# Performance work log

Hardware: AMD Instinct MI355X
Metric: run time of the kernel (lower is better)

## Reference

```python
import jax, jax.numpy as jnp
import numpy as np

# PointCNN layer dims
N, NUM_PTS, P, K, DIMS = 32, 2048, 1024, 16, 3
C_IN, C_OUT = 64, 128
C_HALF = C_OUT // 2            # dense lift of raw features
C_MID = C_OUT // 4             # lifted coord features (C_in != 0)
DM = min(int(np.ceil(C_OUT / C_IN)), 4)   # depth multiplier = 2
C_CAT = C_MID + C_HALF         # 96 channels into X-transform matmul
BN_INV = 1.0 / float(np.sqrt(1.0 + 1e-5))  # inference BN, running mean 0 / var 1


def _dense(x, W, b, g, be):
    # Dense = Linear -> ELU -> BatchNorm (inference affine)
    return g * (jax.nn.elu(x @ W + b) * BN_INV) + be


def setup_inputs() -> dict:
    key = jax.random.key(0)
    ks = jax.random.split(key, 24)
    def rn(k, shape, s=0.1):
        return (jax.random.normal(k, shape) * s).astype(jnp.float32)
    return {
        "rep_pts": jax.random.normal(ks[0], (N, P, DIMS), jnp.float32),
        "pts": jax.random.normal(ks[1], (N, NUM_PTS, DIMS), jnp.float32),
        "fts": jax.random.normal(ks[2], (N, NUM_PTS, C_IN), jnp.float32),
        "pts_idx": jax.random.randint(ks[3], (N, P, K), 0, NUM_PTS, dtype=jnp.int32),
        # PointCNN.dense : C_in -> C_out//2
        "d0_W": rn(ks[4], (C_IN, C_HALF)), "d0_b": rn(ks[5], (C_HALF,)),
        "d0_g": jnp.ones((C_HALF,), jnp.float32), "d0_be": rn(ks[6], (C_HALF,)),
        # XConv.dense1 : dims -> C_mid
        "d1_W": rn(ks[7], (DIMS, C_MID)), "d1_b": rn(ks[8], (C_MID,)),
        "d1_g": jnp.ones((C_MID,), jnp.float32), "d1_be": rn(ks[9], (C_MID,)),
        # XConv.dense2 : C_mid -> C_mid
        "d2_W": rn(ks[10], (C_MID, C_MID)), "d2_b": rn(ks[11], (C_MID,)),
        "d2_g": jnp.ones((C_MID,), jnp.float32), "d2_be": rn(ks[12], (C_MID,)),
        # x_trans: Conv2d(dims -> K*K, kernel (1,K)) then 2 Dense (no BN)
        "xc_W": rn(ks[13], (K * K, DIMS, K)), "xc_b": rn(ks[14], (K * K,)),
        "xd1_W": rn(ks[15], (K * K, K * K)), "xd1_b": rn(ks[16], (K * K,)),
        "xd2_W": rn(ks[17], (K * K, K * K)), "xd2_b": rn(ks[18], (K * K,)),
        # end_conv: depthwise (1,K) conv + pointwise conv + ELU + BN
        "dw_W": rn(ks[19], (C_CAT, DM, K)), "dw_b": rn(ks[20], (C_CAT * DM,)),
        "pw_W": rn(ks[21], (C_CAT * DM, C_OUT)), "pw_b": rn(ks[22], (C_OUT,)),
        "end_g": jnp.ones((C_OUT,), jnp.float32), "end_be": rn(ks[23], (C_OUT,)),
    }


def reference(rep_pts, pts, fts, pts_idx, d0_W, d0_b, d0_g, d0_be,
              d1_W, d1_b, d1_g, d1_be, d2_W, d2_b, d2_g, d2_be,
              xc_W, xc_b, xd1_W, xd1_b, xd2_W, xd2_b,
              dw_W, dw_b, pw_W, pw_b, end_g, end_be):
    # lift raw features: Dense C_in -> C_out//2
    fts_l = _dense(fts, d0_W, d0_b, d0_g, d0_be)          # (N, NUM_PTS, C_half)
    # select_region: per-batch irregular neighbor gather
    gather = jax.vmap(lambda a, i: a[i])
    pts_reg = gather(pts, pts_idx)                        # (N,P,K,dims)
    fts_reg = gather(fts_l, pts_idx)                      # (N,P,K,C_half)
    pts_local = pts_reg - rep_pts[:, :, None, :]          # center on rep point
    # lifting MLP on local coordinates
    h = _dense(pts_local, d1_W, d1_b, d1_g, d1_be)
    h = _dense(h, d2_W, d2_b, d2_g, d2_be)                # (N,P,K,C_mid)
    fts_cat = jnp.concatenate([h, fts_reg], axis=-1)      # (N,P,K,C_cat)
    # learned X-transform: Conv2d(dims->K*K, (1,K)) collapses K -> 1, then 2 Dense
    X = jax.nn.elu(jnp.einsum('npkd,qdk->npq', pts_local, xc_W) + xc_b)
    X = jax.nn.elu(X @ xd1_W + xd1_b)
    X = (X @ xd2_W + xd2_b).reshape(pts.shape[0], P, K, K)
    fts_X = jnp.einsum('npij,npjc->npic', X, fts_cat)     # (N,P,K,C_cat)
    # depthwise (groups=C_cat, kernel (1,K)) -> channel layout c*DM+m
    dw = jnp.einsum('npkc,cmk->npcm', fts_X, dw_W)
    dw = dw.reshape(pts.shape[0], P, C_CAT * DM) + dw_b
    # pointwise conv + ELU + inference BN, squeeze collapsed K axis
    out = jax.nn.elu(dw @ pw_W + pw_b)
    return end_g * (out * BN_INV) + end_be                # (N,P,C_out)
```

## Files before the change

### kernel.cpp

```cpp
#include <hip/hip_runtime.h>
#include <hip/hip_bf16.h>
#include <math.h>

#define NBATCH 32
#define NUMPT 2048
#define PP 1024
#define MPB 16
#define BN_INV 0.9999950000374996f

typedef __attribute__((ext_vector_type(8))) short short8;
typedef __attribute__((ext_vector_type(4))) short short4v;
typedef __attribute__((ext_vector_type(4))) float f32x4;

#define MFMA(a,b,c) __builtin_amdgcn_mfma_f32_16x16x32_bf16(a,b,c,0,0,0)

#define FTSL_ELEMS 4194304
#define OFF_D0F  0
#define OFF_XCF  4096
#define OFF_X1F  20480
#define OFF_X2F  86016
#define OFF_D2F  151552
#define OFF_PWF  152576

#define PB0 4096
#define PB1 16384
#define PB2 81920
#define PB3 147456
#define PB4 148480
#define PB5 173056
#define PB6 177152
#define NDB 512
#define NPREP 660

#define CATP 1552

static __device__ __forceinline__ float eluf(float x) {
    return x > 0.0f ? x : (__expf(x) - 1.0f);
}
static __device__ __forceinline__ short f2bf(float x) {
    union { float f; unsigned u; } v; v.f = x;
    unsigned r = v.u + 0x7FFFu + ((v.u >> 16) & 1u);
    return (short)(r >> 16);
}
static __device__ __forceinline__ int f2bf2i(float a, float b) {
    __hip_bfloat162 h = __float22bfloat162_rn(make_float2(a, b));
    int r; __builtin_memcpy(&r, &h, 4); return r;
}
union U8 { short8 s; int i[4]; };
union U4 { short4v s; int i[2]; };

__global__ __launch_bounds__(256) void k_setup(
    const float* __restrict__ fts, const float* __restrict__ d0W,
    const float* __restrict__ xcW, const float* __restrict__ xd1W,
    const float* __restrict__ xd2W, const float* __restrict__ d2W,
    const float* __restrict__ pwW,
    const float* __restrict__ b, const float* __restrict__ g,
    const float* __restrict__ be,
    short* __restrict__ wf, short* __restrict__ fl)
{
    const int tid = threadIdx.x;
    if (blockIdx.x >= NDB) {
        const int gid = PB0 + (blockIdx.x - NDB) * 256 + tid;
        if (gid >= PB6) return;
        float val; int k, n, nt, off;
        if (gid < PB1) {
            int s = gid - PB0;
            n = s / 48; k = s - n * 48; nt = 16; off = OFF_XCF;
            val = xcW[s];
        } else if (gid < PB2) {
            int s = gid - PB1;
            k = s >> 8; n = s & 255; nt = 16; off = OFF_X1F;
            val = xd1W[s];
        } else if (gid < PB3) {
            int s = gid - PB2;
            k = s >> 8; n = s & 255; nt = 16; off = OFF_X2F;
            val = xd2W[s];
        } else if (gid < PB4) {
            int s = gid - PB3;
            k = s >> 5; n = s & 31; nt = 2; off = OFF_D2F;
            val = d2W[s];
        } else if (gid < PB5) {
            int s = gid - PB4;
            k = s >> 7; n = s & 127; nt = 8; off = OFF_PWF;
            val = pwW[s];
        } else {
            int s = gid - PB5;
            k = 48 + (s >> 8); n = s & 255; nt = 16; off = OFF_XCF;
            val = 0.0f;
        }
        const int dst = off + (((k >> 5) * nt + (n >> 4)) * 64
                               + ((k >> 3) & 3) * 16 + (n & 15)) * 8 + (k & 7);
        wf[dst] = f2bf(val);
        return;
    }

    __shared__ __align__(16) short sB[2 * 4160];
    __shared__ __align__(16) short sW0[4096];
    const long base = (long)blockIdx.x * 128 * 64;

    {
        const int k = tid >> 2, n0 = (tid & 3) * 16;
        #pragma unroll
        for (int i4 = 0; i4 < 4; ++i4) {
            float4 v = *(const float4*)&d0W[k * 64 + n0 + i4 * 4];
            float vv[4] = {v.x, v.y, v.z, v.w};
            #pragma unroll
            for (int u = 0; u < 4; ++u) {
                int n = n0 + i4 * 4 + u;
                sW0[(((k >> 5) * 4 + (n >> 4)) * 64 + ((k >> 3) & 3) * 16 + (n & 15)) * 8 + (k & 7)]
                    = f2bf(vv[u]);
            }
        }
    }

    #pragma unroll
    for (int it = 0; it < 4; ++it) {
        const int gidx = tid + it * 256;
        const int r = gidx >> 3, o = gidx & 7;
        float4 va = *(const float4*)&fts[base + r * 64 + o * 8];
        float4 vb = *(const float4*)&fts[base + r * 64 + o * 8 + 4];
        U8 pk;
        pk.i[0] = f2bf2i(va.x, va.y); pk.i[1] = f2bf2i(va.z, va.w);
        pk.i[2] = f2bf2i(vb.x, vb.y); pk.i[3] = f2bf2i(vb.z, vb.w);
        *(short8*)&sB[(o >> 2) * 4160 + (r >> 4) * 520 + ((o & 3) * 16 + (r & 15)) * 8] = pk.s;
    }
    __syncthreads();

    const int wave = tid >> 6, lane = tid & 63;
    const int col = lane & 15, quad = lane >> 4;
    const f32x4 fz = {0.f, 0.f, 0.f, 0.f};
    f32x4 acc[2][4] = {{fz, fz, fz, fz}, {fz, fz, fz, fz}};
    #pragma unroll
    for (int kt = 0; kt < 2; ++kt) {
        short8 af[4];
        #pragma unroll
        for (int mt = 0; mt < 4; ++mt)
            af[mt] = *(const short8*)&sW0[((kt * 4 + mt) * 64 + lane) * 8];
        #pragma unroll
        for (int ni = 0; ni < 2; ++ni) {
            short8 bf_ = *(const short8*)&sB[kt * 4160 + (wave * 2 + ni) * 520 + lane * 8];
            #pragma unroll
            for (int mt = 0; mt < 4; ++mt)
                acc[ni][mt] = MFMA(af[mt], bf_, acc[ni][mt]);
        }
    }
    #pragma unroll
    for (int mt = 0; mt < 4; ++mt) {
        const int c0 = mt * 16 + quad * 4;
        float4 b4 = *(const float4*)&b[c0];
        float4 g4 = *(const float4*)&g[c0];
        float4 e4 = *(const float4*)&be[c0];
        g4.x *= BN_INV; g4.y *= BN_INV; g4.z *= BN_INV; g4.w *= BN_INV;
        #pragma unroll
        for (int ni = 0; ni < 2; ++ni) {
            long rowg = (long)blockIdx.x * 128 + (wave * 2 + ni) * 16 + col;
            U4 sv;
            sv.i[0] = f2bf2i(g4.x * eluf(acc[ni][mt][0] + b4.x) + e4.x,
                             g4.y * eluf(acc[ni][mt][1] + b4.y) + e4.y);
            sv.i[1] = f2bf2i(g4.z * eluf(acc[ni][mt][2] + b4.z) + e4.z,
                             g4.w * eluf(acc[ni][mt][3] + b4.w) + e4.w);
            *(short4v*)&fl[rowg * 64 + c0] = sv.s;
        }
    }
}

__global__ __launch_bounds__(256) void k_xconv(
    const float* __restrict__ rep_pts, const float* __restrict__ pts,
    const int* __restrict__ pts_idx, const short* __restrict__ fl,
    const short* __restrict__ wf,
    const float* __restrict__ d1W, const float* __restrict__ d1b,
    const float* __restrict__ d1g, const float* __restrict__ d1be,
    const float* __restrict__ d2b, const float* __restrict__ d2g,
    const float* __restrict__ d2be,
    const float* __restrict__ xcb, const float* __restrict__ xd1b,
    const float* __restrict__ xd2b,
    const float* __restrict__ dwW, const float* __restrict__ dwb,
    const float* __restrict__ pwb,
    const float* __restrict__ endg, const float* __restrict__ endbe,
    float* __restrict__ out)
{
    __shared__ __align__(16) short s_catF[MPB * CATP];
    __shared__ __align__(16) short s_big[8448];
    __shared__ __align__(16) short s_X0b[4160];
    __shared__ __align__(16) short s_plF[1024];

    const int tid = threadIdx.x;
    const int wave = tid >> 6, lane = tid & 63;
    const int col = lane & 15, quad = lane >> 4;
    const int n = blockIdx.x >> 6;
    const int pb = (blockIdx.x & 63) * MPB;
    const long prow0 = (long)n * PP + pb;
    short* s_h1F = s_big;
    short* s_X1 = s_big;
    short* s_X2 = s_big + 4160;
    short* s_dwF = s_X0b;
    const f32x4 fz = {0.f, 0.f, 0.f, 0.f};
    const short8 zz = {0, 0, 0, 0, 0, 0, 0, 0};

    for (int i = 768 + tid; i < 1024; i += 256) s_plF[i] = 0;
    const int p0 = tid >> 4, k0 = tid & 15;
    const int idxv = pts_idx[(prow0 + p0) * 16 + k0];
    float x0, x1, x2;
    {
        const float* pp = pts + ((long)n * NUMPT + idxv) * 3;
        const float* rp = rep_pts + (prow0 + p0) * 3;
        x0 = pp[0] - rp[0]; x1 = pp[1] - rp[1]; x2 = pp[2] - rp[2];
        const float v[3] = {x0, x1, x2};
        #pragma unroll
        for (int d = 0; d < 3; ++d) {
            int kk = d * 16 + k0;
            s_plF[((kk >> 5) * 64 + ((kk >> 3) & 3) * 16 + p0) * 8 + (kk & 7)] = f2bf(v[d]);
        }
    }

    short8 gv[8];
    {
        const short8* gp = (const short8*)(fl + ((long)n * NUMPT + idxv) * 64);
        #pragma unroll
        for (int i = 0; i < 8; ++i) gv[i] = gp[i];
    }

    #pragma unroll
    for (int oct = 0; oct < 4; ++oct) {
        U8 v8;
        float zv[8];
        #pragma unroll
        for (int u = 0; u < 8; ++u) {
            int c = oct * 8 + u;
            float z = d1b[c] + x0 * d1W[c] + x1 * d1W[32 + c] + x2 * d1W[64 + c];
            zv[u] = (d1g[c] * BN_INV) * eluf(z) + d1be[c];
        }
        v8.i[0] = f2bf2i(zv[0], zv[1]); v8.i[1] = f2bf2i(zv[2], zv[3]);
        v8.i[2] = f2bf2i(zv[4], zv[5]); v8.i[3] = f2bf2i(zv[6], zv[7]);
        *(short8*)&s_h1F[(p0 * 66 + oct * 16 + k0) * 8] = v8.s;
    }

    {
        const int gbase = p0 * CATP + 32 * 16 + k0;
        #pragma unroll
        for (int i = 0; i < 8; ++i) {
            #pragma unroll
            for (int u = 0; u < 8; ++u)
                s_catF[gbase + (i * 8 + u) * 16] = gv[i][u];
        }
    }
    __syncthreads();

    {
        const short8* B = (const short8*)(wf + OFF_D2F);
        short8 b0 = B[lane], b1 = B[64 + lane];
        short8 a[4];
        #pragma unroll
        for (int mt0 = 0; mt0 < 4; ++mt0)
            a[mt0] = *(const short8*)&s_h1F[((wave * 4 + mt0) * 66 + lane) * 8];
        #pragma unroll
        for (int nb = 0; nb < 2; ++nb) {
            int c2 = nb * 16 + col;
            float bb = d2b[c2], gg = d2g[c2] * BN_INV, bee = d2be[c2];
            #pragma unroll
            for (int mt0 = 0; mt0 < 4; ++mt0) {
                int mt = wave * 4 + mt0;
                f32x4 acc = MFMA(a[mt0], nb ? b1 : b0, fz);
                U4 sv;
                sv.i[0] = f2bf2i(gg * eluf(acc[0] + bb) + bee,
                                 gg * eluf(acc[1] + bb) + bee);
                sv.i[1] = f2bf2i(gg * eluf(acc[2] + bb) + bee,
                                 gg * eluf(acc[3] + bb) + bee);
                *(short4v*)&s_catF[mt * CATP + c2 * 16 + quad * 4] = sv.s;
            }
        }
    }

    {
        short8 a0 = *(const short8*)&s_plF[lane * 8];
        short8 a1 = *(const short8*)&s_plF[(64 + lane) * 8];
        const short8* B = (const short8*)(wf + OFF_XCF);
        #pragma unroll
        for (int t = 0; t < 4; ++t) {
            int nb = wave * 4 + t;
            f32x4 acc = MFMA(a0, B[nb * 64 + lane], fz);
            acc = MFMA(a1, B[(16 + nb) * 64 + lane], acc);
            int q = nb * 16 + col;
            float bq = xcb[q];
            #pragma unroll
            for (int r = 0; r < 4; ++r) {
                int p = quad * 4 + r;
                s_X0b[(q >> 5) * 520 + (((q >> 3) & 3) * 16 + p) * 8 + (q & 7)]
                    = f2bf(eluf(acc[r] + bq));
            }
        }
    }
    __syncthreads();

    {
        short8 a[8];
        #pragma unroll
        for (int kt = 0; kt < 8; ++kt)
            a[kt] = *(const short8*)&s_X0b[kt * 520 + lane * 8];
        const short8* B = (const short8*)(wf + OFF_X1F);
        #pragma unroll
        for (int t = 0; t < 4; ++t) {
            int nb = wave * 4 + t;
            f32x4 acc = fz;
            #pragma unroll
            for (int kt = 0; kt < 8; ++kt)
                acc = MFMA(a[kt], B[(kt * 16 + nb) * 64 + lane], acc);
            int q = nb * 16 + col;
            float bq = xd1b[q];
            #pragma unroll
            for (int r = 0; r < 4; ++r) {
                int p = quad * 4 + r;
                s_X1[(q >> 5) * 520 + (((q >> 3) & 3) * 16 + p) * 8 + (q & 7)]
                    = f2bf(eluf(acc[r] + bq));
            }
        }
    }
    __syncthreads();

    {
        short8 a[8];
        #pragma unroll
        for (int kt = 0; kt < 8; ++kt)
            a[kt] = *(const short8*)&s_X1[kt * 520 + lane * 8];
        const short8* B = (const short8*)(wf + OFF_X2F);
        #pragma unroll
        for (int t = 0; t < 4; ++t) {
            int nb = wave * 4 + t;
            f32x4 acc = fz;
            #pragma unroll
            for (int kt = 0; kt < 8; ++kt)
                acc = MFMA(a[kt], B[(kt * 16 + nb) * 64 + lane], acc);
            float bq = xd2b[nb * 16 + col];
            #pragma unroll
            for (int r = 0; r < 4; ++r) {
                int p = quad * 4 + r;
                s_X2[p * 264 + ((col >> 3) * 16 + nb) * 8 + (col & 7)] = f2bf(acc[r] + bq);
            }
        }
    }
    __syncthreads();

    {
        float4 wd0[6], wd1[6]; float2 bdw[6];
        #pragma unroll
        for (int nb = 0; nb < 6; ++nb) {
            int c = nb * 16 + col;
            wd0[nb] = *(const float4*)&dwW[(c * 2 + 0) * 16 + quad * 4];
            wd1[nb] = *(const float4*)&dwW[(c * 2 + 1) * 16 + quad * 4];
            bdw[nb] = *(const float2*)&dwb[c * 2];
        }
        #pragma unroll
        for (int pi = 0; pi < 4; ++pi) {
            int p = wave * 4 + pi;
            short8 afr = zz;
            if (lane < 32) afr = *(const short8*)&s_X2[p * 264 + lane * 8];
            #pragma unroll
            for (int nb = 0; nb < 6; ++nb) {
                short8 bfr = zz;
                if (lane < 32)
                    bfr = *(const short8*)&s_catF[p * CATP + (nb * 16 + col) * 16 + quad * 8];
                f32x4 acc = MFMA(afr, bfr, fz);
                float q0 = acc[0] * wd0[nb].x + acc[1] * wd0[nb].y + acc[2] * wd0[nb].z + acc[3] * wd0[nb].w;
                float q1 = acc[0] * wd1[nb].x + acc[1] * wd1[nb].y + acc[2] * wd1[nb].z + acc[3] * wd1[nb].w;
                q0 += __shfl_xor(q0, 16); q0 += __shfl_xor(q0, 32);
                q1 += __shfl_xor(q1, 16); q1 += __shfl_xor(q1, 32);
                if (quad == 0) {
                    int c2 = col * 2;
                    int ad = (nb * 64 + (c2 >> 3) * 16 + p) * 8 + (c2 & 7);
                    *(int*)&s_dwF[ad] = f2bf2i(q0 + bdw[nb].x, q1 + bdw[nb].y);
                }
            }
        }
    }
    __syncthreads();

    {
        short8 a[6];
        #pragma unroll
        for (int kt = 0; kt < 6; ++kt)
            a[kt] = *(const short8*)&s_dwF[(kt * 64 + lane) * 8];
        const short8* B = (const short8*)(wf + OFF_PWF);
        #pragma unroll
        for (int t = 0; t < 2; ++t) {
            int nb = wave * 2 + t;
            f32x4 acc = fz;
            #pragma unroll
            for (int kt = 0; kt < 6; ++kt)
                acc = MFMA(a[kt], B[(kt * 8 + nb) * 64 + lane], acc);
            int o = nb * 16 + col;
            float bo = pwb[o], go = endg[o] * BN_INV, beo = endbe[o];
            #pragma unroll
            for (int r = 0; r < 4; ++r) {
                int p = quad * 4 + r;
                out[(prow0 + p) * 128 + o] = go * eluf(acc[r] + bo) + beo;
            }
        }
    }
}

extern "C" void kernel_launch(void* const* d_in, const int* in_sizes, int n_in,
                              void* d_out, int out_size, void* d_ws, size_t ws_size,
                              hipStream_t stream) {
    const float* rep_pts = (const float*)d_in[0];
    const float* pts     = (const float*)d_in[1];
    const float* fts     = (const float*)d_in[2];
    const int*   pts_idx = (const int*)d_in[3];
    const float* d0W = (const float*)d_in[4];
    const float* d0b = (const float*)d_in[5];
    const float* d0g = (const float*)d_in[6];
    const float* d0be = (const float*)d_in[7];
    const float* d1W = (const float*)d_in[8];
    const float* d1b = (const float*)d_in[9];
    const float* d1g = (const float*)d_in[10];
    const float* d1be = (const float*)d_in[11];
    const float* d2W = (const float*)d_in[12];
    const float* d2b = (const float*)d_in[13];
    const float* d2g = (const float*)d_in[14];
    const float* d2be = (const float*)d_in[15];
    const float* xcW = (const float*)d_in[16];
    const float* xcb = (const float*)d_in[17];
    const float* xd1W = (const float*)d_in[18];
    const float* xd1b = (const float*)d_in[19];
    const float* xd2W = (const float*)d_in[20];
    const float* xd2b = (const float*)d_in[21];
    const float* dwW = (const float*)d_in[22];
    const float* dwb = (const float*)d_in[23];
    const float* pwW = (const float*)d_in[24];
    const float* pwb = (const float*)d_in[25];
    const float* endg = (const float*)d_in[26];
    const float* endbe = (const float*)d_in[27];
    float* out = (float*)d_out;

    short* wsS = (short*)d_ws;
    short* fl = wsS;
    short* wf = wsS + FTSL_ELEMS;

    k_setup<<<NDB + NPREP, 256, 0, stream>>>(
        fts, d0W, xcW, xd1W, xd2W, d2W, pwW, d0b, d0g, d0be, wf, fl);
    k_xconv<<<NBATCH * (PP / MPB), 256, 0, stream>>>(
        rep_pts, pts, pts_idx, fl, wf,
        d1W, d1b, d1g, d1be, d2b, d2g, d2be,
        xcb, xd1b, xd2b, dwW, dwb, pwb, endg, endbe, out);
}
```

Before: 200.3 us.

## Double xconv block to 512 threads, splitting per-point work across eight waves

The fused X-conv kernel now runs with 512 threads (eight waves) per 16-point block instead of 256. Each gather row is split between two threads, each loading half of the 64 lifted feature channels and computing half of the dense1 octets. Each MFMA stage now gives every wave half as many tiles as before. The dense2 matmul also moves after the x_trans conv so the two share one barrier. This aims to raise latency hiding and occupancy, at the cost of more threads, more barrier participants and possibly tighter register budgets under launch_bounds(512,4).

```diff
diff --git a/kernel.cpp b/kernel.cpp
--- a/kernel.cpp
+++ b/kernel.cpp
@@ -164,7 +164,7 @@
     }
 }
 
-__global__ __launch_bounds__(256) void k_xconv(
+__global__ __launch_bounds__(512, 4) void k_xconv(
     const float* __restrict__ rep_pts, const float* __restrict__ pts,
     const int* __restrict__ pts_idx, const short* __restrict__ fl,
     const short* __restrict__ wf,
@@ -197,31 +197,35 @@
     const f32x4 fz = {0.f, 0.f, 0.f, 0.f};
     const short8 zz = {0, 0, 0, 0, 0, 0, 0, 0};
 
-    for (int i = 768 + tid; i < 1024; i += 256) s_plF[i] = 0;
-    const int p0 = tid >> 4, k0 = tid & 15;
+    if (tid < 256) s_plF[768 + tid] = 0;
+    const int row = tid >> 1, half = tid & 1;
+    const int p0 = row >> 4, k0 = row & 15;
     const int idxv = pts_idx[(prow0 + p0) * 16 + k0];
     float x0, x1, x2;
     {
         const float* pp = pts + ((long)n * NUMPT + idxv) * 3;
         const float* rp = rep_pts + (prow0 + p0) * 3;
         x0 = pp[0] - rp[0]; x1 = pp[1] - rp[1]; x2 = pp[2] - rp[2];
-        const float v[3] = {x0, x1, x2};
-        #pragma unroll
-        for (int d = 0; d < 3; ++d) {
-            int kk = d * 16 + k0;
-            s_plF[((kk >> 5) * 64 + ((kk >> 3) & 3) * 16 + p0) * 8 + (kk & 7)] = f2bf(v[d]);
-        }
-    }
-
-    short8 gv[8];
-    {
-        const short8* gp = (const short8*)(fl + ((long)n * NUMPT + idxv) * 64);
-        #pragma unroll
-        for (int i = 0; i < 8; ++i) gv[i] = gp[i];
+        if (half == 0) {
+            const float v[3] = {x0, x1, x2};
+            #pragma unroll
+            for (int d = 0; d < 3; ++d) {
+                int kk = d * 16 + k0;
+                s_plF[((kk >> 5) * 64 + ((kk >> 3) & 3) * 16 + p0) * 8 + (kk & 7)] = f2bf(v[d]);
+            }
+        }
+    }
+
+    short8 gv[4];
+    {
+        const short8* gp = (const short8*)(fl + ((long)n * NUMPT + idxv) * 64 + half * 32);
+        #pragma unroll
+        for (int i = 0; i < 4; ++i) gv[i] = gp[i];
     }
 
     #pragma unroll
-    for (int oct = 0; oct < 4; ++oct) {
+    for (int j = 0; j < 2; ++j) {
+        const int oct = half * 2 + j;
         U8 v8;
         float zv[8];
         #pragma unroll
@@ -236,48 +240,23 @@
     }
 
     {
-        const int gbase = p0 * CATP + 32 * 16 + k0;
-        #pragma unroll
-        for (int i = 0; i < 8; ++i) {
+        const int gbase = p0 * CATP + (32 + half * 32) * 16 + k0;
+        #pragma unroll
+        for (int i = 0; i < 4; ++i) {
             #pragma unroll
             for (int u = 0; u < 8; ++u)
                 s_catF[gbase + (i * 8 + u) * 16] = gv[i][u];
         }
     }
     __syncthreads();
-
-    {
-        const short8* B = (const short8*)(wf + OFF_D2F);
-        short8 b0 = B[lane], b1 = B[64 + lane];
-        short8 a[4];
-        #pragma unroll
-        for (int mt0 = 0; mt0 < 4; ++mt0)
-            a[mt0] = *(const short8*)&s_h1F[((wave * 4 + mt0) * 66 + lane) * 8];
-        #pragma unroll
-        for (int nb = 0; nb < 2; ++nb) {
-            int c2 = nb * 16 + col;
-            float bb = d2b[c2], gg = d2g[c2] * BN_INV, bee = d2be[c2];
-            #pragma unroll
-            for (int mt0 = 0; mt0 < 4; ++mt0) {
-                int mt = wave * 4 + mt0;
-                f32x4 acc = MFMA(a[mt0], nb ? b1 : b0, fz);
-                U4 sv;
-                sv.i[0] = f2bf2i(gg * eluf(acc[0] + bb) + bee,
-                                 gg * eluf(acc[1] + bb) + bee);
-                sv.i[1] = f2bf2i(gg * eluf(acc[2] + bb) + bee,
-                                 gg * eluf(acc[3] + bb) + bee);
-                *(short4v*)&s_catF[mt * CATP + c2 * 16 + quad * 4] = sv.s;
-            }
-        }
-    }
 
     {
         short8 a0 = *(const short8*)&s_plF[lane * 8];
         short8 a1 = *(const short8*)&s_plF[(64 + lane) * 8];
         const short8* B = (const short8*)(wf + OFF_XCF);
         #pragma unroll
-        for (int t = 0; t < 4; ++t) {
-            int nb = wave * 4 + t;
+        for (int t = 0; t < 2; ++t) {
+            int nb = wave * 2 + t;
             f32x4 acc = MFMA(a0, B[nb * 64 + lane], fz);
             acc = MFMA(a1, B[(16 + nb) * 64 + lane], acc);
             int q = nb * 16 + col;
@@ -290,6 +269,26 @@
             }
         }
     }
+
+    {
+        const short8* B = (const short8*)(wf + OFF_D2F);
+        const int nb = wave & 1, mtb = (wave >> 1) * 4;
+        short8 bfr = B[nb * 64 + lane];
+        const int c2 = nb * 16 + col;
+        const float bb = d2b[c2], gg = d2g[c2] * BN_INV, bee = d2be[c2];
+        #pragma unroll
+        for (int mt0 = 0; mt0 < 4; ++mt0) {
+            int mt = mtb + mt0;
+            short8 a = *(const short8*)&s_h1F[(mt * 66 + lane) * 8];
+            f32x4 acc = MFMA(a, bfr, fz);
+            U4 sv;
+            sv.i[0] = f2bf2i(gg * eluf(acc[0] + bb) + bee,
+                             gg * eluf(acc[1] + bb) + bee);
+            sv.i[1] = f2bf2i(gg * eluf(acc[2] + bb) + bee,
+                             gg * eluf(acc[3] + bb) + bee);
+            *(short4v*)&s_catF[mt * CATP + c2 * 16 + quad * 4] = sv.s;
+        }
+    }
     __syncthreads();
 
     {
@@ -299,8 +298,8 @@
             a[kt] = *(const short8*)&s_X0b[kt * 520 + lane * 8];
         const short8* B = (const short8*)(wf + OFF_X1F);
         #pragma unroll
-        for (int t = 0; t < 4; ++t) {
-            int nb = wave * 4 + t;
+        for (int t = 0; t < 2; ++t) {
+            int nb = wave * 2 + t;
             f32x4 acc = fz;
             #pragma unroll
             for (int kt = 0; kt < 8; ++kt)
@@ -324,8 +323,8 @@
             a[kt] = *(const short8*)&s_X1[kt * 520 + lane * 8];
         const short8* B = (const short8*)(wf + OFF_X2F);
         #pragma unroll
-        for (int t = 0; t < 4; ++t) {
-            int nb = wave * 4 + t;
+        for (int t = 0; t < 2; ++t) {
+            int nb = wave * 2 + t;
             f32x4 acc = fz;
             #pragma unroll
             for (int kt = 0; kt < 8; ++kt)
@@ -350,8 +349,8 @@
             bdw[nb] = *(const float2*)&dwb[c * 2];
         }
         #pragma unroll
-        for (int pi = 0; pi < 4; ++pi) {
-            int p = wave * 4 + pi;
+        for (int pi = 0; pi < 2; ++pi) {
+            int p = wave * 2 + pi;
             short8 afr = zz;
             if (lane < 32) afr = *(const short8*)&s_X2[p * 264 + lane * 8];
             #pragma unroll
@@ -380,20 +379,17 @@
         for (int kt = 0; kt < 6; ++kt)
             a[kt] = *(const short8*)&s_dwF[(kt * 64 + lane) * 8];
         const short8* B = (const short8*)(wf + OFF_PWF);
-        #pragma unroll
-        for (int t = 0; t < 2; ++t) {
-            int nb = wave * 2 + t;
-            f32x4 acc = fz;
-            #pragma unroll
-            for (int kt = 0; kt < 6; ++kt)
-                acc = MFMA(a[kt], B[(kt * 8 + nb) * 64 + lane], acc);
-            int o = nb * 16 + col;
-            float bo = pwb[o], go = endg[o] * BN_INV, beo = endbe[o];
-            #pragma unroll
-            for (int r = 0; r < 4; ++r) {
-                int p = quad * 4 + r;
-                out[(prow0 + p) * 128 + o] = go * eluf(acc[r] + bo) + beo;
-            }
+        const int nb = wave;
+        f32x4 acc = fz;
+        #pragma unroll
+        for (int kt = 0; kt < 6; ++kt)
+            acc = MFMA(a[kt], B[(kt * 8 + nb) * 64 + lane], acc);
+        const int o = nb * 16 + col;
+        const float bo = pwb[o], go = endg[o] * BN_INV, beo = endbe[o];
+        #pragma unroll
+        for (int r = 0; r < 4; ++r) {
+            int p = quad * 4 + r;
+            out[(prow0 + p) * 128 + o] = go * eluf(acc[r] + bo) + beo;
         }
     }
 }
@@ -437,7 +433,7 @@
 
     k_setup<<<NDB + NPREP, 256, 0, stream>>>(
         fts, d0W, xcW, xd1W, xd2W, d2W, pwW, d0b, d0g, d0be, wf, fl);
-    k_xconv<<<NBATCH * (PP / MPB), 256, 0, stream>>>(
+    k_xconv<<<NBATCH * (PP / MPB), 512, 0, stream>>>(
         rep_pts, pts, pts_idx, fl, wf,
         d1W, d1b, d1g, d1be, d2b, d2g, d2be,
         xcb, xd1b, xd2b, dwW, dwb, pwb, endg, endbe, out);
```

Result: no change. 203.5 us (+1.6%).
